# Kernel tuning notes

Measured on AMD Instinct MI355X. Metric: run time of the kernel, lower is better.

Reference implementation:

```python
import jax, jax.numpy as jnp
import numpy as np

RANK = 32
ALPHA = 1.0
SCALE = ALPHA / RANK


def setup_inputs() -> dict:
    key = jax.random.key(0)
    k1, k2, k3, k4, k5 = jax.random.split(key, 5)
    B_, S, D_in, D_out = 4, 2048, 4096, 4096
    x = jax.random.normal(k1, (B_, S, D_in), dtype=jnp.float32)
    # nn.Linear weight: [out, in], kaiming-ish scale
    W = jax.random.normal(k2, (D_out, D_in), dtype=jnp.float32) / np.sqrt(D_in)
    bias = jax.random.normal(k3, (D_out,), dtype=jnp.float32) * 0.01
    A = jax.random.normal(k4, (D_in, RANK), dtype=jnp.float32) * 0.01
    # torch init is zeros for B; use small random so output depends on LoRA path
    Bm = jax.random.normal(k5, (RANK, D_out), dtype=jnp.float32) * 0.01
    return {"x": x, "W": W, "bias": bias, "A": A, "B": Bm}


def reference(x, W, bias, A, B):
    # Original: y = x @ (W + scale*(A@B)^T)^T + bias
    # Mathematically identical fused form (two GEMMs, no [in,out] delta):
    base = jnp.einsum('bsd,od->bso', x, W)          # [B,S,out]
    lora = jnp.einsum('bsr,ro->bso', x @ A, B)       # [B,S,rank]->[B,S,out]
    return base + SCALE * lora + bias
```

## Files before the change

### kernel.cpp

```cpp
#include <hip/hip_runtime.h>
#include <hip/hip_bf16.h>
#include <stdint.h>

#define RANK 32
#define SCALE (1.0f / 32.0f)

typedef __bf16 bf16x8 __attribute__((ext_vector_type(8)));
typedef float f32x4 __attribute__((ext_vector_type(4)));

__device__ __forceinline__ void gload16(const void* g, void* l) {
  __builtin_amdgcn_global_load_lds(
      (const __attribute__((address_space(1))) unsigned int*)g,
      (__attribute__((address_space(3))) unsigned int*)l, 16, 0, 0);
}

__device__ __forceinline__ unsigned short f2bf(float f) {
  __hip_bfloat16 h = __float2bfloat16(f);
  return *reinterpret_cast<unsigned short*>(&h);
}

__global__ __launch_bounds__(256) void transpose_B_k(const float* __restrict__ B,
                                                     float* __restrict__ Bt,
                                                     int Dout) {
  int idx = blockIdx.x * 256 + threadIdx.x;
  int r = idx / Dout;
  int o = idx - r * Dout;
  Bt[(long long)o * RANK + r] = B[idx];
}

__global__ __launch_bounds__(256) void merge_W_k(const float* __restrict__ W,
                                                 const float* __restrict__ A,
                                                 const float* __restrict__ Bt,
                                                 unsigned short* __restrict__ Wbf,
                                                 int Din, int Dout) {
  __shared__ float sB[16 * RANK];
  int nib = Din / 256;
  int ib = blockIdx.x % nib;
  int ob = blockIdx.x / nib;
  int i0 = ib * 256, o0 = ob * 16;
  int t = threadIdx.x;

  if (t < 128) {
    reinterpret_cast<float4*>(sB)[t] =
        reinterpret_cast<const float4*>(Bt + (long long)o0 * RANK)[t];
  }

  float a[RANK];
  const float4* Ap = reinterpret_cast<const float4*>(A + (long long)(i0 + t) * RANK);
#pragma unroll
  for (int c = 0; c < RANK / 4; ++c) {
    float4 v = Ap[c];
    a[c * 4 + 0] = v.x; a[c * 4 + 1] = v.y;
    a[c * 4 + 2] = v.z; a[c * 4 + 3] = v.w;
  }
  __syncthreads();

  int i = i0 + t;
  int KB = Din / 32;
  long long fragrow = (long long)(o0 >> 4) * KB + (i >> 5);
  int slot_base = ((i & 31) >> 3) * 16;
  int e = i & 7;

  for (int o = 0; o < 16; ++o) {
    float d = 0.f;
#pragma unroll
    for (int j = 0; j < RANK; ++j) d += a[j] * sB[o * RANK + j];
    long long off = (long long)(o0 + o) * Din + i;
    float w = __builtin_nontemporal_load(&W[off]);
    Wbf[fragrow * 512 + (slot_base + o) * 8 + e] = f2bf(w + SCALE * d);
  }
}

__global__ __launch_bounds__(256) void cast_x_k(const float* __restrict__ in,
                                                unsigned short* __restrict__ out,
                                                long long n8) {
  long long i = (long long)blockIdx.x * 256 + threadIdx.x;
  if (i >= n8) return;
  const f32x4* in4 = reinterpret_cast<const f32x4*>(in) + i * 2;
  f32x4 v0 = __builtin_nontemporal_load(in4);
  f32x4 v1 = __builtin_nontemporal_load(in4 + 1);
  union { unsigned short u[8]; uint4 q; } p;
  p.u[0] = f2bf(v0.x); p.u[1] = f2bf(v0.y); p.u[2] = f2bf(v0.z); p.u[3] = f2bf(v0.w);
  p.u[4] = f2bf(v1.x); p.u[5] = f2bf(v1.y); p.u[6] = f2bf(v1.z); p.u[7] = f2bf(v1.w);
  reinterpret_cast<uint4*>(out)[i] = p.q;
}

__device__ __forceinline__ void stage1(const unsigned short* g, int K, int koff,
                                       int row0, unsigned short* ldsbase,
                                       int t, int wid) {
  int r = t >> 2;
  int cg = (t & 3) ^ ((r ^ (r >> 2)) & 3);
  gload16(g + (long long)(row0 + r) * K + koff + cg * 8,
          ldsbase + row0 * 32 + wid * 512);
}

__device__ __forceinline__ int swz_off32(int rowl, int k) {
  return rowl * 32 + ((((k) >> 3) ^ ((rowl ^ (rowl >> 2)) & 3)) << 3);
}

__global__ __launch_bounds__(512, 2) void gemm256_bias_k(
    const unsigned short* __restrict__ Xb,
    const unsigned short* __restrict__ Wbf,
    const float* __restrict__ bias,
    float* __restrict__ Out,
    int M, int N, int K) {
  __shared__ unsigned short As[2][256 * 32];

  int nbn = N / 256;
  int cpx = gridDim.x >> 3;
  int bid = blockIdx.x;
  int xcd = bid & 7, local = bid >> 3;
  int bm, bn;
  int mrows = cpx / nbn;
  if (mrows * nbn == cpx) {
    bn = local / mrows;
    bm = xcd * mrows + (local - bn * mrows);
  } else {
    int swz = xcd * cpx + local;
    bm = swz / nbn; bn = swz % nbn;
  }

  int t = threadIdx.x;
  int wid = t >> 6, lane = t & 63;
  int wr = wid >> 2, wc = wid & 3;
  int lr = lane & 15, kq = (lane >> 4) * 8;
  int wr64 = wr * 64, wc32 = wc * 32;

  const unsigned short* ga = Xb + (long long)bm * 256 * K;
  const int KB = K / 32;
  const unsigned short* gbf = Wbf + ((long long)(bn * 16 + wc * 2) * KB) * 512
                                  + lane * 8;

  f32x4 acc[8][4] = {};
  bf16x8 aL0[4], aL1[4], aH0[4], aH1[4], Bv0[4], Bv1[4];

#define LDA(BUF, ROWBASE) \
  (*(const bf16x8*)&As[BUF][swz_off32((ROWBASE) + lr, kq)])

#define GATE(NSTR) \
  asm volatile("s_waitcnt vmcnt(" NSTR ")" ::: "memory"); \
  __builtin_amdgcn_s_barrier();

#define READ_AH(AH, BUF) \
  AH[0] = LDA(BUF, 128 + wr64);      AH[1] = LDA(BUF, 128 + wr64 + 16); \
  AH[2] = LDA(BUF, 128 + wr64 + 32); AH[3] = LDA(BUF, 128 + wr64 + 48);

#define READ_AL(AL, BUF) \
  AL[0] = LDA(BUF, wr64);      AL[1] = LDA(BUF, wr64 + 16); \
  AL[2] = LDA(BUF, wr64 + 32); AL[3] = LDA(BUF, wr64 + 48);

#define LOADB(BV, T) { \
  const unsigned short* fb = gbf + (long long)(T) * 512;               \
  BV[0] = *(const bf16x8*)(fb);                                        \
  BV[1] = *(const bf16x8*)(fb + (long long)KB * 512);                  \
  BV[2] = *(const bf16x8*)(fb + (long long)8 * KB * 512);              \
  BV[3] = *(const bf16x8*)(fb + (long long)9 * KB * 512); }

#define MFMA16(AF, BF, MO)                                                   \
  __builtin_amdgcn_sched_barrier(0);                                         \
  __builtin_amdgcn_s_setprio(1);                                             \
  _Pragma("unroll")                                                          \
  for (int m = 0; m < 4; ++m)                                                \
    _Pragma("unroll")                                                        \
    for (int n = 0; n < 4; ++n)                                              \
      acc[(MO) + m][n] = __builtin_amdgcn_mfma_f32_16x16x32_bf16(            \
          AF[m], BF[n], acc[(MO) + m][n], 0, 0, 0);                          \
  __builtin_amdgcn_s_setprio(0);

  stage1(ga, K, 0, 0,    &As[0][0], t, wid);
  stage1(ga, K, 0, 128,  &As[0][0], t, wid);
  LOADB(Bv0, 0)
  stage1(ga, K, 32, 0,   &As[1][0], t, wid);
  asm volatile("s_waitcnt vmcnt(1)" ::: "memory");
  __builtin_amdgcn_s_barrier();
  READ_AL(aL0, 0)

  for (int j = 0; j < 63; ++j) {
    int ko = j * 64;
    GATE("1")
    stage1(ga, K, ko + 32, 128, &As[1][0], t, wid);
    LOADB(Bv1, 2 * j + 1)
    READ_AH(aH0, 0)
    MFMA16(aL0, Bv0, 0)
    GATE("5")
    stage1(ga, K, ko + 64, 0, &As[0][0], t, wid);
    READ_AL(aL1, 1)
    MFMA16(aH0, Bv0, 4)
    GATE("1")
    stage1(ga, K, ko + 64, 128, &As[0][0], t, wid);
    LOADB(Bv0, 2 * j + 2)
    READ_AH(aH1, 1)
    MFMA16(aL1, Bv1, 0)
    GATE("5")
    stage1(ga, K, ko + 96, 0, &As[1][0], t, wid);
    READ_AL(aL0, 0)
    MFMA16(aH1, Bv1, 4)
  }

  GATE("1")
  stage1(ga, K, 127 * 32, 128, &As[1][0], t, wid);
  LOADB(Bv1, 127)
  READ_AH(aH0, 0)
  MFMA16(aL0, Bv0, 0)
  GATE("5")
  READ_AL(aL1, 1)
  MFMA16(aH0, Bv0, 4)
  GATE("0")
  READ_AH(aH1, 1)
  MFMA16(aL1, Bv1, 0)
  MFMA16(aH1, Bv1, 4)

#undef LDA
#undef GATE
#undef READ_AH
#undef READ_AL
#undef LOADB
#undef MFMA16

  int rq = (lane >> 4) * 4;
#pragma unroll
  for (int n = 0; n < 4; ++n) {
    int gc = bn * 256 + (n >= 2 ? 128 : 0) + wc32 + (n & 1) * 16 + lr;
    float bv = bias[gc];
#pragma unroll
    for (int m = 0; m < 8; ++m) {
      long long gr = (long long)bm * 256 + (m >= 4 ? 128 : 0) + wr64 + (m & 3) * 16 + rq;
#pragma unroll
      for (int v = 0; v < 4; ++v)
        __builtin_nontemporal_store(acc[m][n][v] + bv, &Out[(gr + v) * N + gc]);
    }
  }
}

extern "C" void kernel_launch(void* const* d_in, const int* in_sizes, int n_in,
                              void* d_out, int out_size, void* d_ws, size_t ws_size,
                              hipStream_t stream) {
  const float* x    = (const float*)d_in[0];
  const float* W    = (const float*)d_in[1];
  const float* bias = (const float*)d_in[2];
  const float* A    = (const float*)d_in[3];
  const float* B    = (const float*)d_in[4];

  int Din  = in_sizes[3] / RANK;
  int Dout = in_sizes[4] / RANK;
  long long M = (long long)in_sizes[0] / Din;

  size_t xb_bytes = (size_t)M * Din * 2;
  size_t wb_bytes = (size_t)Dout * Din * 2;
  size_t bt_bytes = (size_t)Dout * RANK * 4;
  if (ws_size < xb_bytes + wb_bytes + bt_bytes) return;

  char* ws = (char*)d_ws;
  unsigned short* Xb  = (unsigned short*)ws;
  unsigned short* Wbf = (unsigned short*)(ws + xb_bytes);
  float* Bt           = (float*)(ws + xb_bytes + wb_bytes);

  transpose_B_k<<<dim3((Dout * RANK) / 256), dim3(256), 0, stream>>>(B, Bt, Dout);
  merge_W_k<<<dim3((Dout / 16) * (Din / 256)), dim3(256), 0, stream>>>(W, A, Bt, Wbf, Din, Dout);
  long long n8 = M * Din / 8;
  cast_x_k<<<dim3((unsigned)(n8 / 256)), dim3(256), 0, stream>>>(x, Xb, n8);
  gemm256_bias_k<<<dim3((unsigned)((M / 256) * (Dout / 256))), dim3(512), 0, stream>>>(
      Xb, Wbf, bias, (float*)d_out, (int)M, Dout, Din);
}
```

Measured before the change: 329.5 us.

## Switch GEMM to 32x32x16 MFMA with matching pre-packed weight fragment layout

Replaces the 16x16x32 bf16 MFMA tiles with 32x32x16 MFMA. The packed-weight layout written by the prep kernel, the B fragment loads, the LDS A-fragment reads and the epilogue store mapping are all changed to match. Larger MFMA tiles should cut the number of LDS reads and instructions per FLOP and raise matrix-core throughput. The cost is a different register footprint and a less coalesced output write pattern.

```diff
diff --git a/kernel.cpp b/kernel.cpp
--- a/kernel.cpp
+++ b/kernel.cpp
@@ -7,6 +7,7 @@
 
 typedef __bf16 bf16x8 __attribute__((ext_vector_type(8)));
 typedef float f32x4 __attribute__((ext_vector_type(4)));
+typedef float f32x16 __attribute__((ext_vector_type(16)));
 
 __device__ __forceinline__ void gload16(const void* g, void* l) {
   __builtin_amdgcn_global_load_lds(
@@ -56,18 +57,20 @@
   __syncthreads();
 
   int i = i0 + t;
-  int KB = Din / 32;
-  long long fragrow = (long long)(o0 >> 4) * KB + (i >> 5);
-  int slot_base = ((i & 31) >> 3) * 16;
+  int KB16 = Din >> 4;
+  int kb = i >> 4;
+  int lhalf = ((i >> 3) & 1) * 32;
   int e = i & 7;
 
   for (int o = 0; o < 16; ++o) {
     float d = 0.f;
 #pragma unroll
     for (int j = 0; j < RANK; ++j) d += a[j] * sB[o * RANK + j];
-    long long off = (long long)(o0 + o) * Din + i;
+    int oo = o0 + o;
+    long long off = (long long)oo * Din + i;
     float w = __builtin_nontemporal_load(&W[off]);
-    Wbf[fragrow * 512 + (slot_base + o) * 8 + e] = f2bf(w + SCALE * d);
+    long long dst = (((long long)(oo >> 5) * KB16 + kb) * 64 + (lhalf + (oo & 31))) * 8 + e;
+    Wbf[dst] = f2bf(w + SCALE * d);
   }
 }
 
@@ -123,48 +126,51 @@
   int t = threadIdx.x;
   int wid = t >> 6, lane = t & 63;
   int wr = wid >> 2, wc = wid & 3;
-  int lr = lane & 15, kq = (lane >> 4) * 8;
-  int wr64 = wr * 64, wc32 = wc * 32;
+  int lr32 = lane & 31, kq32 = (lane >> 5) * 8;
+  int wr64 = wr * 64;
 
   const unsigned short* ga = Xb + (long long)bm * 256 * K;
-  const int KB = K / 32;
-  const unsigned short* gbf = Wbf + ((long long)(bn * 16 + wc * 2) * KB) * 512
+  const int KB16 = K >> 4;
+  const unsigned short* gbf = Wbf + ((long long)(bn * 8 + wc * 2) * KB16) * 512
                                   + lane * 8;
 
-  f32x4 acc[8][4] = {};
-  bf16x8 aL0[4], aL1[4], aH0[4], aH1[4], Bv0[4], Bv1[4];
-
-#define LDA(BUF, ROWBASE) \
-  (*(const bf16x8*)&As[BUF][swz_off32((ROWBASE) + lr, kq)])
+  f32x16 acc[4][2] = {};
+  bf16x8 aL0[2][2], aL1[2][2], aH0[2][2], aH1[2][2], Bv0[4], Bv1[4];
+
+#define LDA32(BUF, ROWBASE, KH) \
+  (*(const bf16x8*)&As[BUF][swz_off32((ROWBASE) + lr32, (KH) * 16 + kq32)])
 
 #define GATE(NSTR) \
   asm volatile("s_waitcnt vmcnt(" NSTR ")" ::: "memory"); \
   __builtin_amdgcn_s_barrier();
 
 #define READ_AH(AH, BUF) \
-  AH[0] = LDA(BUF, 128 + wr64);      AH[1] = LDA(BUF, 128 + wr64 + 16); \
-  AH[2] = LDA(BUF, 128 + wr64 + 32); AH[3] = LDA(BUF, 128 + wr64 + 48);
+  AH[0][0] = LDA32(BUF, 128 + wr64, 0);      AH[0][1] = LDA32(BUF, 128 + wr64, 1); \
+  AH[1][0] = LDA32(BUF, 128 + wr64 + 32, 0); AH[1][1] = LDA32(BUF, 128 + wr64 + 32, 1);
 
 #define READ_AL(AL, BUF) \
-  AL[0] = LDA(BUF, wr64);      AL[1] = LDA(BUF, wr64 + 16); \
-  AL[2] = LDA(BUF, wr64 + 32); AL[3] = LDA(BUF, wr64 + 48);
+  AL[0][0] = LDA32(BUF, wr64, 0);      AL[0][1] = LDA32(BUF, wr64, 1); \
+  AL[1][0] = LDA32(BUF, wr64 + 32, 0); AL[1][1] = LDA32(BUF, wr64 + 32, 1);
 
 #define LOADB(BV, T) { \
-  const unsigned short* fb = gbf + (long long)(T) * 512;               \
+  const unsigned short* fb = gbf + (long long)(T) * 1024;              \
   BV[0] = *(const bf16x8*)(fb);                                        \
-  BV[1] = *(const bf16x8*)(fb + (long long)KB * 512);                  \
-  BV[2] = *(const bf16x8*)(fb + (long long)8 * KB * 512);              \
-  BV[3] = *(const bf16x8*)(fb + (long long)9 * KB * 512); }
-
-#define MFMA16(AF, BF, MO)                                                   \
+  BV[1] = *(const bf16x8*)(fb + 512);                                  \
+  BV[2] = *(const bf16x8*)(fb + (long long)KB16 * 512);                \
+  BV[3] = *(const bf16x8*)(fb + (long long)KB16 * 512 + 512); }
+
+#define MFMA8(AF, BF, MO)                                                    \
   __builtin_amdgcn_sched_barrier(0);                                         \
   __builtin_amdgcn_s_setprio(1);                                             \
   _Pragma("unroll")                                                          \
-  for (int m = 0; m < 4; ++m)                                                \
+  for (int mb = 0; mb < 2; ++mb)                                             \
     _Pragma("unroll")                                                        \
-    for (int n = 0; n < 4; ++n)                                              \
-      acc[(MO) + m][n] = __builtin_amdgcn_mfma_f32_16x16x32_bf16(            \
-          AF[m], BF[n], acc[(MO) + m][n], 0, 0, 0);                          \
+    for (int n = 0; n < 2; ++n) {                                            \
+      acc[(MO) + mb][n] = __builtin_amdgcn_mfma_f32_32x32x16_bf16(           \
+          AF[mb][0], BF[n * 2], acc[(MO) + mb][n], 0, 0, 0);                 \
+      acc[(MO) + mb][n] = __builtin_amdgcn_mfma_f32_32x32x16_bf16(           \
+          AF[mb][1], BF[n * 2 + 1], acc[(MO) + mb][n], 0, 0, 0);             \
+    }                                                                        \
   __builtin_amdgcn_s_setprio(0);
 
   stage1(ga, K, 0, 0,    &As[0][0], t, wid);
@@ -181,53 +187,55 @@
     stage1(ga, K, ko + 32, 128, &As[1][0], t, wid);
     LOADB(Bv1, 2 * j + 1)
     READ_AH(aH0, 0)
-    MFMA16(aL0, Bv0, 0)
+    MFMA8(aL0, Bv0, 0)
     GATE("5")
     stage1(ga, K, ko + 64, 0, &As[0][0], t, wid);
     READ_AL(aL1, 1)
-    MFMA16(aH0, Bv0, 4)
+    MFMA8(aH0, Bv0, 2)
     GATE("1")
     stage1(ga, K, ko + 64, 128, &As[0][0], t, wid);
     LOADB(Bv0, 2 * j + 2)
     READ_AH(aH1, 1)
-    MFMA16(aL1, Bv1, 0)
+    MFMA8(aL1, Bv1, 0)
     GATE("5")
     stage1(ga, K, ko + 96, 0, &As[1][0], t, wid);
     READ_AL(aL0, 0)
-    MFMA16(aH1, Bv1, 4)
+    MFMA8(aH1, Bv1, 2)
   }
 
   GATE("1")
   stage1(ga, K, 127 * 32, 128, &As[1][0], t, wid);
   LOADB(Bv1, 127)
   READ_AH(aH0, 0)
-  MFMA16(aL0, Bv0, 0)
+  MFMA8(aL0, Bv0, 0)
   GATE("5")
   READ_AL(aL1, 1)
-  MFMA16(aH0, Bv0, 4)
+  MFMA8(aH0, Bv0, 2)
   GATE("0")
   READ_AH(aH1, 1)
-  MFMA16(aL1, Bv1, 0)
-  MFMA16(aH1, Bv1, 4)
-
-#undef LDA
+  MFMA8(aL1, Bv1, 0)
+  MFMA8(aH1, Bv1, 2)
+
+#undef LDA32
 #undef GATE
 #undef READ_AH
 #undef READ_AL
 #undef LOADB
-#undef MFMA16
-
-  int rq = (lane >> 4) * 4;
-#pragma unroll
-  for (int n = 0; n < 4; ++n) {
-    int gc = bn * 256 + (n >= 2 ? 128 : 0) + wc32 + (n & 1) * 16 + lr;
-    float bv = bias[gc];
-#pragma unroll
-    for (int m = 0; m < 8; ++m) {
-      long long gr = (long long)bm * 256 + (m >= 4 ? 128 : 0) + wr64 + (m & 3) * 16 + rq;
-#pragma unroll
-      for (int v = 0; v < 4; ++v)
-        __builtin_nontemporal_store(acc[m][n][v] + bv, &Out[(gr + v) * N + gc]);
+#undef MFMA8
+
+  int rq5 = 4 * (lane >> 5);
+#pragma unroll
+  for (int mq = 0; mq < 4; ++mq) {
+    long long grb = (long long)bm * 256 + (mq >= 2 ? 128 : 0) + wr64 + (mq & 1) * 32 + rq5;
+#pragma unroll
+    for (int n = 0; n < 2; ++n) {
+      int gc = bn * 256 + wc * 64 + n * 32 + lr32;
+      float bv = bias[gc];
+#pragma unroll
+      for (int r = 0; r < 16; ++r) {
+        long long gr = grb + (r & 3) + 8 * (r >> 2);
+        __builtin_nontemporal_store(acc[mq][n][r] + bv, &Out[gr * N + gc]);
+      }
     }
   }
 }
```

Result: slower. 342.6 us (+4.0%).

## Triple-buffer A tiles in LDS with full-K-step phases and deeper prefetch

Applied to the files above, without the earlier changes.

Moves the A-tile LDS staging from two buffers to three. Each phase now prefetches the tile two K-steps ahead, reads a full 256-row fragment set, and issues 32 MFMAs per barrier instead of the previous half-tile interleave. This halves the number of barriers per K-step and gives global loads more time to land. In exchange, LDS use rises to 48KB per block, which may limit the two-blocks-per-CU occupancy, and fragment register pressure increases.

```diff
diff --git a/kernel.cpp b/kernel.cpp
--- a/kernel.cpp
+++ b/kernel.cpp
@@ -104,7 +104,7 @@
     const float* __restrict__ bias,
     float* __restrict__ Out,
     int M, int N, int K) {
-  __shared__ unsigned short As[2][256 * 32];
+  __shared__ unsigned short As[3][256 * 32];
 
   int nbn = N / 256;
   int cpx = gridDim.x >> 3;
@@ -132,7 +132,7 @@
                                   + lane * 8;
 
   f32x4 acc[8][4] = {};
-  bf16x8 aL0[4], aL1[4], aH0[4], aH1[4], Bv0[4], Bv1[4];
+  bf16x8 aF0[8], aF1[8], Bv0[4], Bv1[4];
 
 #define LDA(BUF, ROWBASE) \
   (*(const bf16x8*)&As[BUF][swz_off32((ROWBASE) + lr, kq)])
@@ -141,13 +141,11 @@
   asm volatile("s_waitcnt vmcnt(" NSTR ")" ::: "memory"); \
   __builtin_amdgcn_s_barrier();
 
-#define READ_AH(AH, BUF) \
-  AH[0] = LDA(BUF, 128 + wr64);      AH[1] = LDA(BUF, 128 + wr64 + 16); \
-  AH[2] = LDA(BUF, 128 + wr64 + 32); AH[3] = LDA(BUF, 128 + wr64 + 48);
-
-#define READ_AL(AL, BUF) \
-  AL[0] = LDA(BUF, wr64);      AL[1] = LDA(BUF, wr64 + 16); \
-  AL[2] = LDA(BUF, wr64 + 32); AL[3] = LDA(BUF, wr64 + 48);
+#define READ_AF(AF, BUF) \
+  AF[0] = LDA(BUF, wr64);            AF[1] = LDA(BUF, wr64 + 16); \
+  AF[2] = LDA(BUF, wr64 + 32);       AF[3] = LDA(BUF, wr64 + 48); \
+  AF[4] = LDA(BUF, 128 + wr64);      AF[5] = LDA(BUF, 128 + wr64 + 16); \
+  AF[6] = LDA(BUF, 128 + wr64 + 32); AF[7] = LDA(BUF, 128 + wr64 + 48);
 
 #define LOADB(BV, T) { \
   const unsigned short* fb = gbf + (long long)(T) * 512;               \
@@ -156,66 +154,66 @@
   BV[2] = *(const bf16x8*)(fb + (long long)8 * KB * 512);              \
   BV[3] = *(const bf16x8*)(fb + (long long)9 * KB * 512); }
 
-#define MFMA16(AF, BF, MO)                                                   \
+#define MFMA32(AF, BF)                                                       \
   __builtin_amdgcn_sched_barrier(0);                                         \
   __builtin_amdgcn_s_setprio(1);                                             \
   _Pragma("unroll")                                                          \
-  for (int m = 0; m < 4; ++m)                                                \
+  for (int m = 0; m < 8; ++m)                                                \
     _Pragma("unroll")                                                        \
     for (int n = 0; n < 4; ++n)                                              \
-      acc[(MO) + m][n] = __builtin_amdgcn_mfma_f32_16x16x32_bf16(            \
-          AF[m], BF[n], acc[(MO) + m][n], 0, 0, 0);                          \
+      acc[m][n] = __builtin_amdgcn_mfma_f32_16x16x32_bf16(                   \
+          AF[m], BF[n], acc[m][n], 0, 0, 0);                                 \
   __builtin_amdgcn_s_setprio(0);
 
-  stage1(ga, K, 0, 0,    &As[0][0], t, wid);
-  stage1(ga, K, 0, 128,  &As[0][0], t, wid);
+#define PH(AFU, AFN, BVU, BVN, RB, SB, XX, DOST)                             \
+  GATE("2")                                                                  \
+  LOADB(BVN, (XX) + 1)                                                       \
+  if (DOST) {                                                                \
+    stage1(ga, K, ((XX) + 3) * 32, 0,   &As[SB][0], t, wid);                 \
+    stage1(ga, K, ((XX) + 3) * 32, 128, &As[SB][0], t, wid);                 \
+  }                                                                          \
+  READ_AF(AFN, RB)                                                           \
+  MFMA32(AFU, BVU)
+
+  stage1(ga, K, 0,  0,   &As[0][0], t, wid);
+  stage1(ga, K, 0,  128, &As[0][0], t, wid);
+  stage1(ga, K, 32, 0,   &As[1][0], t, wid);
+  stage1(ga, K, 32, 128, &As[1][0], t, wid);
   LOADB(Bv0, 0)
-  stage1(ga, K, 32, 0,   &As[1][0], t, wid);
-  asm volatile("s_waitcnt vmcnt(1)" ::: "memory");
+  stage1(ga, K, 64, 0,   &As[2][0], t, wid);
+  stage1(ga, K, 64, 128, &As[2][0], t, wid);
+  asm volatile("s_waitcnt vmcnt(8)" ::: "memory");
   __builtin_amdgcn_s_barrier();
-  READ_AL(aL0, 0)
-
-  for (int j = 0; j < 63; ++j) {
-    int ko = j * 64;
-    GATE("1")
-    stage1(ga, K, ko + 32, 128, &As[1][0], t, wid);
-    LOADB(Bv1, 2 * j + 1)
-    READ_AH(aH0, 0)
-    MFMA16(aL0, Bv0, 0)
-    GATE("5")
-    stage1(ga, K, ko + 64, 0, &As[0][0], t, wid);
-    READ_AL(aL1, 1)
-    MFMA16(aH0, Bv0, 4)
-    GATE("1")
-    stage1(ga, K, ko + 64, 128, &As[0][0], t, wid);
-    LOADB(Bv0, 2 * j + 2)
-    READ_AH(aH1, 1)
-    MFMA16(aL1, Bv1, 0)
-    GATE("5")
-    stage1(ga, K, ko + 96, 0, &As[1][0], t, wid);
-    READ_AL(aL0, 0)
-    MFMA16(aH1, Bv1, 4)
-  }
-
-  GATE("1")
-  stage1(ga, K, 127 * 32, 128, &As[1][0], t, wid);
+  READ_AF(aF0, 0)
+
+  for (int k = 0; k < 20; ++k) {
+    int X = 6 * k;
+    PH(aF0, aF1, Bv0, Bv1, 1, 0, X + 0, 1)
+    PH(aF1, aF0, Bv1, Bv0, 2, 1, X + 1, 1)
+    PH(aF0, aF1, Bv0, Bv1, 0, 2, X + 2, 1)
+    PH(aF1, aF0, Bv1, Bv0, 1, 0, X + 3, 1)
+    PH(aF0, aF1, Bv0, Bv1, 2, 1, X + 4, 1)
+    PH(aF1, aF0, Bv1, Bv0, 0, 2, X + 5, 1)
+  }
+  PH(aF0, aF1, Bv0, Bv1, 1, 0, 120, 1)
+  PH(aF1, aF0, Bv1, Bv0, 2, 1, 121, 1)
+  PH(aF0, aF1, Bv0, Bv1, 0, 2, 122, 1)
+  PH(aF1, aF0, Bv1, Bv0, 1, 0, 123, 1)
+  PH(aF0, aF1, Bv0, Bv1, 2, 1, 124, 1)
+  PH(aF1, aF0, Bv1, Bv0, 0, 2, 125, 0)
+  GATE("0")
   LOADB(Bv1, 127)
-  READ_AH(aH0, 0)
-  MFMA16(aL0, Bv0, 0)
-  GATE("5")
-  READ_AL(aL1, 1)
-  MFMA16(aH0, Bv0, 4)
+  READ_AF(aF1, 1)
+  MFMA32(aF0, Bv0)
   GATE("0")
-  READ_AH(aH1, 1)
-  MFMA16(aL1, Bv1, 0)
-  MFMA16(aH1, Bv1, 4)
+  MFMA32(aF1, Bv1)
 
 #undef LDA
 #undef GATE
-#undef READ_AH
-#undef READ_AL
+#undef READ_AF
 #undef LOADB
-#undef MFMA16
+#undef MFMA32
+#undef PH
 
   int rq = (lane >> 4) * 4;
 #pragma unroll
```

After: 387.9 us. 17.7% more time.
